# Optimization experiments

Measured on AMD Instinct MI355X. Metric: run time of the kernel, lower is better.

Reference implementation:

```python
import jax, jax.numpy as jnp
import numpy as np

N = 100000
E = 1600000
H = 8
D_IN = 128
D_HEAD = 16  # output_dim // n_heads


def setup_inputs() -> dict:
    key = jax.random.key(0)
    ks = jax.random.split(key, 8)
    x = jax.random.normal(ks[0], (N, D_IN), dtype=jnp.float32)
    W = jax.random.normal(ks[1], (H, D_IN, D_HEAD), dtype=jnp.float32) * 0.05
    a1 = jax.random.normal(ks[2], (H, D_HEAD), dtype=jnp.float32) * 0.1
    b1 = jnp.zeros((H,), dtype=jnp.float32)
    a2 = jax.random.normal(ks[3], (H, D_HEAD), dtype=jnp.float32) * 0.1
    b2 = jnp.zeros((H,), dtype=jnp.float32)
    src = jnp.sort(jax.random.randint(ks[4], (E,), 0, N)).astype(jnp.int32)
    dst = jax.random.randint(ks[5], (E,), 0, N).astype(jnp.int32)
    return {"x": x, "W": W, "a1": a1, "b1": b1, "a2": a2, "b2": b2,
            "src": src, "dst": dst}


def _gat_forward(x, W, a1, b1, a2, b2, src, dst):
    n = x.shape[0]
    # per-head linear transform: [H, N, D_HEAD]
    feats = jnp.einsum('nd,hdo->hno', x, W)
    # per-node attention scalars (1x1 conv with bias): [H, N]
    f1 = jnp.einsum('hno,ho->hn', feats, a1) + b1[:, None]
    f2 = jnp.einsum('hno,ho->hn', feats, a2) + b2[:, None]
    # edge logits: logit[e] = f1[src[e]] + f2[dst[e]]  -> [E, H]
    e = f1[:, src].T + f2[:, dst].T
    e = jnp.maximum(0.2 * e, e)  # leaky_relu
    # sparse row-softmax over each source node's neighbors (segment softmax)
    m = jax.ops.segment_max(e, src, num_segments=n)           # [N, H]
    ex = jnp.exp(e - m[src])                                   # [E, H]
    denom = jax.ops.segment_sum(ex, src, num_segments=n)      # [N, H]
    coef = ex / denom[src]                                     # [E, H]
    # spmm: out[i] = sum_{j in N(i)} coef[ij] * feats[j]
    feats_nhd = jnp.transpose(feats, (1, 0, 2))                # [N, H, D_HEAD]
    msg = coef[:, :, None] * feats_nhd[dst]                    # [E, H, D_HEAD]
    out = jax.ops.segment_sum(msg, src, num_segments=n)       # [N, H, D_HEAD]
    out = out.reshape(n, H * D_HEAD)
    return jax.nn.elu(out)


def reference(x, W, a1, b1, a2, b2, src, dst):
    return _gat_forward(x, W, a1, b1, a2, b2, src, dst)
```

## Files before the change

### kernel.cpp

```cpp
#include <hip/hip_runtime.h>
#include <hip/hip_bf16.h>
#include <math.h>

#define HEADS 8
#define D_IN 128
#define D_HEAD 16
#define D_OUT 128

typedef unsigned short ushort_t;
typedef unsigned int uint_t;
typedef __attribute__((ext_vector_type(8))) short short8;
typedef __attribute__((ext_vector_type(4))) float floatx4;

static __device__ inline uint_t f32_to_bf16(float f) {
    uint_t u = __float_as_uint(f);
    return (u + 0x7fffu + ((u >> 16) & 1u)) >> 16;
}
static __device__ inline uint_t pack_bf16(float lo, float hi) {
    return (f32_to_bf16(hi) << 16) | f32_to_bf16(lo);
}
static __device__ inline float bf_lo(uint_t p) { return __uint_as_float(p << 16); }
static __device__ inline float bf_hi(uint_t p) { return __uint_as_float(p & 0xffff0000u); }

__global__ __launch_bounds__(256) void wprep_kernel(
    const float* __restrict__ Wg, ushort_t* __restrict__ Wbt)
{
    int i = blockIdx.x * 256 + threadIdx.x;
    int c = i >> 7, d = i & 127;
    float v = Wg[(size_t)(c >> 4) * (D_IN * D_HEAD) + d * D_HEAD + (c & 15)];
    Wbt[i] = (ushort_t)f32_to_bf16(v);
}

__global__ __launch_bounds__(256) void gemm_feats_mfma(
    const float* __restrict__ x, const ushort_t* __restrict__ Wbt,
    const float* __restrict__ a1, const float* __restrict__ b1,
    const float* __restrict__ a2, const float* __restrict__ b2,
    ushort_t* __restrict__ feats, float* __restrict__ f1,
    float* __restrict__ f2, int n)
{
    __shared__ ushort_t Xs[64][136];

    const int tid  = threadIdx.x;
    const int wave = tid >> 6;
    const int lane = tid & 63;
    const int row0 = blockIdx.x * 64;

    {
        const int r  = tid >> 2;
        const int c0 = (tid & 3) * 32;
        const bool valid = (row0 + r) < n;
        const float* xr = x + (size_t)(row0 + r) * D_IN + c0;
        uint_t buf[16];
#pragma unroll
        for (int q = 0; q < 8; ++q) {
            float4 v = make_float4(0.f, 0.f, 0.f, 0.f);
            if (valid) v = *(const float4*)(xr + q * 4);
            buf[2 * q]     = pack_bf16(v.x, v.y);
            buf[2 * q + 1] = pack_bf16(v.z, v.w);
        }
        uint4* dp = (uint4*)&Xs[r][c0];
#pragma unroll
        for (int q = 0; q < 4; ++q)
            dp[q] = make_uint4(buf[4 * q], buf[4 * q + 1], buf[4 * q + 2], buf[4 * q + 3]);
    }
    __syncthreads();

    const int m  = lane & 15;
    const int kg = lane >> 4;

    floatx4 acc[8];
#pragma unroll
    for (int ct = 0; ct < 8; ++ct) acc[ct] = (floatx4){0.f, 0.f, 0.f, 0.f};

#pragma unroll
    for (int ks = 0; ks < 4; ++ks) {
        short8 xb = *(const short8*)&Xs[16 * wave + m][ks * 32 + kg * 8];
#pragma unroll
        for (int ct = 0; ct < 8; ++ct) {
            short8 wa = *(const short8*)(Wbt + (size_t)(ct * 16 + m) * D_IN + ks * 32 + kg * 8);
            acc[ct] = __builtin_amdgcn_mfma_f32_16x16x32_bf16(wa, xb, acc[ct], 0, 0, 0);
        }
    }

    const int node = row0 + wave * 16 + m;
    const bool valid = node < n;

    if (valid) {
#pragma unroll
        for (int ct = 0; ct < 8; ++ct) {
            uint_t lo = pack_bf16(acc[ct][0], acc[ct][1]);
            uint_t hi = pack_bf16(acc[ct][2], acc[ct][3]);
            *(uint2*)(feats + (size_t)node * D_OUT + ct * 16 + kg * 4) = make_uint2(lo, hi);
        }
    }

#pragma unroll
    for (int ct = 0; ct < 8; ++ct) {
        float p1 = 0.f, p2 = 0.f;
#pragma unroll
        for (int r = 0; r < 4; ++r) {
            const int o = kg * 4 + r;
            p1 = fmaf(acc[ct][r], a1[ct * D_HEAD + o], p1);
            p2 = fmaf(acc[ct][r], a2[ct * D_HEAD + o], p2);
        }
        p1 += __shfl_xor(p1, 16); p1 += __shfl_xor(p1, 32);
        p2 += __shfl_xor(p2, 16); p2 += __shfl_xor(p2, 32);
        if (kg == 0 && valid) {
            f1[(size_t)node * HEADS + ct] = p1 + b1[ct];
            f2[(size_t)node * HEADS + ct] = p2 + b2[ct];
        }
    }
}

__global__ __launch_bounds__(256) void rowptr_kernel(
    const int* __restrict__ src, int* __restrict__ row_ptr, int n, int e)
{
    int i = blockIdx.x * blockDim.x + threadIdx.x;
    if (i > n) return;
    int lo = 0, hi = e;
    while (lo < hi) {
        int mid = (lo + hi) >> 1;
        if (src[mid] < i) lo = mid + 1; else hi = mid;
    }
    row_ptr[i] = lo;
}

__global__ __launch_bounds__(256) void aggregate_kernel(
    const int* __restrict__ row_ptr, const int* __restrict__ dst,
    const ushort_t* __restrict__ feats,
    const float* __restrict__ f1, const float* __restrict__ f2,
    float* __restrict__ out, int n)
{
    int node = blockIdx.x * 4 + (threadIdx.x >> 6);
    node = __builtin_amdgcn_readfirstlane(node);
    if (node >= n) return;
    const int lane = threadIdx.x & 63;
    const int h = lane >> 3;

    const float f1v   = f1[(size_t)node * HEADS + h];
    const int   start = row_ptr[node];
    const int   end   = row_ptr[node + 1];

    const float*    f2h = f2 + h;
    const ushort_t* fl  = feats + 2 * lane;

    float s = 0.f, ax = 0.f, ay = 0.f;
    int e = start;
    for (; e + 4 <= end; e += 4) {
        const int d0 = dst[e], d1 = dst[e + 1], d2 = dst[e + 2], d3 = dst[e + 3];
        const float g0 = f2h[d0 * HEADS], g1 = f2h[d1 * HEADS];
        const float g2 = f2h[d2 * HEADS], g3 = f2h[d3 * HEADS];
        const uint_t p0 = *(const uint_t*)(fl + d0 * D_OUT);
        const uint_t p1 = *(const uint_t*)(fl + d1 * D_OUT);
        const uint_t p2 = *(const uint_t*)(fl + d2 * D_OUT);
        const uint_t p3 = *(const uint_t*)(fl + d3 * D_OUT);
        float z0 = f1v + g0; z0 = fmaxf(z0, 0.2f * z0);
        float z1 = f1v + g1; z1 = fmaxf(z1, 0.2f * z1);
        float z2 = f1v + g2; z2 = fmaxf(z2, 0.2f * z2);
        float z3 = f1v + g3; z3 = fmaxf(z3, 0.2f * z3);
        const float w0 = __expf(z0), w1 = __expf(z1), w2 = __expf(z2), w3 = __expf(z3);
        s += (w0 + w1) + (w2 + w3);
        ax = fmaf(w0, bf_lo(p0), ax); ay = fmaf(w0, bf_hi(p0), ay);
        ax = fmaf(w1, bf_lo(p1), ax); ay = fmaf(w1, bf_hi(p1), ay);
        ax = fmaf(w2, bf_lo(p2), ax); ay = fmaf(w2, bf_hi(p2), ay);
        ax = fmaf(w3, bf_lo(p3), ax); ay = fmaf(w3, bf_hi(p3), ay);
    }
    for (; e < end; ++e) {
        const int d = dst[e];
        const float g = f2h[d * HEADS];
        const uint_t p = *(const uint_t*)(fl + d * D_OUT);
        float z = f1v + g; z = fmaxf(z, 0.2f * z);
        const float w = __expf(z);
        s += w;
        ax = fmaf(w, bf_lo(p), ax); ay = fmaf(w, bf_hi(p), ay);
    }

    float rx = 0.f, ry = 0.f;
    if (end > start) {
        rx = ax / s;
        ry = ay / s;
        rx = rx > 0.f ? rx : expm1f(rx);
        ry = ry > 0.f ? ry : expm1f(ry);
    }
    *(float2*)(out + (size_t)node * D_OUT + 2 * lane) = make_float2(rx, ry);
}

extern "C" void kernel_launch(void* const* d_in, const int* in_sizes, int n_in,
                              void* d_out, int out_size, void* d_ws, size_t ws_size,
                              hipStream_t stream)
{
    const float* x  = (const float*)d_in[0];
    const float* W  = (const float*)d_in[1];
    const float* a1 = (const float*)d_in[2];
    const float* b1 = (const float*)d_in[3];
    const float* a2 = (const float*)d_in[4];
    const float* b2 = (const float*)d_in[5];
    const int* src  = (const int*)d_in[6];
    const int* dst  = (const int*)d_in[7];
    float* out = (float*)d_out;

    const int n = in_sizes[0] / D_IN;
    const int e = in_sizes[6];

    char* ws = (char*)d_ws;
    size_t off = 0;
    ushort_t* feats = (ushort_t*)(ws + off);
    off += (size_t)n * D_OUT * sizeof(ushort_t); off = (off + 255) & ~(size_t)255;
    float* f1 = (float*)(ws + off);
    off += (size_t)n * HEADS * sizeof(float);    off = (off + 255) & ~(size_t)255;
    float* f2 = (float*)(ws + off);
    off += (size_t)n * HEADS * sizeof(float);    off = (off + 255) & ~(size_t)255;
    int* row_ptr = (int*)(ws + off);
    off += (size_t)(n + 1) * sizeof(int);        off = (off + 255) & ~(size_t)255;
    ushort_t* Wbt = (ushort_t*)(ws + off);

    dim3 blk(256);
    wprep_kernel<<<dim3(64), blk, 0, stream>>>(W, Wbt);
    rowptr_kernel<<<dim3((n + 1 + 255) / 256), blk, 0, stream>>>(src, row_ptr, n, e);
    gemm_feats_mfma<<<dim3((n + 63) / 64), blk, 0, stream>>>(
        x, Wbt, a1, b1, a2, b2, feats, f1, f2, n);
    aggregate_kernel<<<dim3((n + 3) / 4), blk, 0, stream>>>(
        row_ptr, dst, feats, f1, f2, out, n);
}
```

Measured before the change: 239.3 us.

## Merge prep kernels, pre-swizzle W fragments, widen GEMM tile, unroll gather by 8

Merges the weight-conversion and row-pointer kernels into one launch, which saves a kernel launch. W is now stored in MFMA fragment order, so each lane's weight load is one contiguous 16-byte read. The GEMM block now covers 128 rows with two accumulator tiles per wave, so each weight fragment is reused twice; x staging is made fully coalesced and a1/a2 are loaded as float4. The aggregation loop is unrolled to 8 edges to keep more gathers in flight, at the cost of more registers.

Measured after the change: 220.9 us. 1.08x faster.

```diff
diff --git a/kernel.cpp b/kernel.cpp
--- a/kernel.cpp
+++ b/kernel.cpp
@@ -22,107 +22,107 @@
 static __device__ inline float bf_lo(uint_t p) { return __uint_as_float(p << 16); }
 static __device__ inline float bf_hi(uint_t p) { return __uint_as_float(p & 0xffff0000u); }
 
-__global__ __launch_bounds__(256) void wprep_kernel(
-    const float* __restrict__ Wg, ushort_t* __restrict__ Wbt)
-{
-    int i = blockIdx.x * 256 + threadIdx.x;
-    int c = i >> 7, d = i & 127;
-    float v = Wg[(size_t)(c >> 4) * (D_IN * D_HEAD) + d * D_HEAD + (c & 15)];
-    Wbt[i] = (ushort_t)f32_to_bf16(v);
+#define PREP_WBLOCKS 64
+__global__ __launch_bounds__(256) void prep_kernel(
+    const float* __restrict__ Wg, ushort_t* __restrict__ Wfrag,
+    const int* __restrict__ src, int* __restrict__ row_ptr, int n, int e)
+{
+    if (blockIdx.x < PREP_WBLOCKS) {
+        int t = blockIdx.x * 256 + threadIdx.x;
+        int j    = t & 7;
+        int lane = (t >> 3) & 63;
+        int ks   = (t >> 9) & 3;
+        int ct   = t >> 11;
+        int k = ks * 32 + (lane >> 4) * 8 + j;
+        int m = lane & 15;
+        float v = Wg[(size_t)ct * (D_IN * D_HEAD) + k * D_HEAD + m];
+        Wfrag[t] = (ushort_t)f32_to_bf16(v);
+    } else {
+        int i = (blockIdx.x - PREP_WBLOCKS) * 256 + threadIdx.x;
+        if (i > n) return;
+        int lo = 0, hi = e;
+        while (lo < hi) {
+            int mid = (lo + hi) >> 1;
+            if (src[mid] < i) lo = mid + 1; else hi = mid;
+        }
+        row_ptr[i] = lo;
+    }
 }
 
 __global__ __launch_bounds__(256) void gemm_feats_mfma(
-    const float* __restrict__ x, const ushort_t* __restrict__ Wbt,
+    const float* __restrict__ x, const ushort_t* __restrict__ Wfrag,
     const float* __restrict__ a1, const float* __restrict__ b1,
     const float* __restrict__ a2, const float* __restrict__ b2,
     ushort_t* __restrict__ feats, float* __restrict__ f1,
     float* __restrict__ f2, int n)
 {
-    __shared__ ushort_t Xs[64][136];
+    __shared__ ushort_t Xs[128][136];
 
     const int tid  = threadIdx.x;
     const int wave = tid >> 6;
     const int lane = tid & 63;
-    const int row0 = blockIdx.x * 64;
-
-    {
-        const int r  = tid >> 2;
-        const int c0 = (tid & 3) * 32;
-        const bool valid = (row0 + r) < n;
-        const float* xr = x + (size_t)(row0 + r) * D_IN + c0;
-        uint_t buf[16];
-#pragma unroll
-        for (int q = 0; q < 8; ++q) {
-            float4 v = make_float4(0.f, 0.f, 0.f, 0.f);
-            if (valid) v = *(const float4*)(xr + q * 4);
-            buf[2 * q]     = pack_bf16(v.x, v.y);
-            buf[2 * q + 1] = pack_bf16(v.z, v.w);
-        }
-        uint4* dp = (uint4*)&Xs[r][c0];
-#pragma unroll
-        for (int q = 0; q < 4; ++q)
-            dp[q] = make_uint4(buf[4 * q], buf[4 * q + 1], buf[4 * q + 2], buf[4 * q + 3]);
+    const int row0 = blockIdx.x * 128;
+
+#pragma unroll
+    for (int it = 0; it < 16; ++it) {
+        int idx = it * 256 + tid;
+        int r   = idx >> 5;
+        int c4  = (idx & 31) * 4;
+        float4 v = make_float4(0.f, 0.f, 0.f, 0.f);
+        if (row0 + r < n) v = *(const float4*)(x + (size_t)(row0 + r) * D_IN + c4);
+        *(uint2*)&Xs[r][c4] = make_uint2(pack_bf16(v.x, v.y), pack_bf16(v.z, v.w));
     }
     __syncthreads();
 
     const int m  = lane & 15;
     const int kg = lane >> 4;
 
-    floatx4 acc[8];
-#pragma unroll
-    for (int ct = 0; ct < 8; ++ct) acc[ct] = (floatx4){0.f, 0.f, 0.f, 0.f};
+    floatx4 acc[2][8];
+#pragma unroll
+    for (int nt = 0; nt < 2; ++nt)
+#pragma unroll
+        for (int ct = 0; ct < 8; ++ct) acc[nt][ct] = (floatx4){0.f, 0.f, 0.f, 0.f};
 
 #pragma unroll
     for (int ks = 0; ks < 4; ++ks) {
-        short8 xb = *(const short8*)&Xs[16 * wave + m][ks * 32 + kg * 8];
+        short8 xb0 = *(const short8*)&Xs[wave * 32 + m][ks * 32 + kg * 8];
+        short8 xb1 = *(const short8*)&Xs[wave * 32 + 16 + m][ks * 32 + kg * 8];
 #pragma unroll
         for (int ct = 0; ct < 8; ++ct) {
-            short8 wa = *(const short8*)(Wbt + (size_t)(ct * 16 + m) * D_IN + ks * 32 + kg * 8);
-            acc[ct] = __builtin_amdgcn_mfma_f32_16x16x32_bf16(wa, xb, acc[ct], 0, 0, 0);
-        }
-    }
-
-    const int node = row0 + wave * 16 + m;
-    const bool valid = node < n;
-
-    if (valid) {
+            short8 wa = *(const short8*)(Wfrag + ((size_t)(ct * 4 + ks) * 64 + lane) * 8);
+            acc[0][ct] = __builtin_amdgcn_mfma_f32_16x16x32_bf16(wa, xb0, acc[0][ct], 0, 0, 0);
+            acc[1][ct] = __builtin_amdgcn_mfma_f32_16x16x32_bf16(wa, xb1, acc[1][ct], 0, 0, 0);
+        }
+    }
+
+#pragma unroll
+    for (int nt = 0; nt < 2; ++nt) {
+        const int node = row0 + wave * 32 + nt * 16 + m;
+        const bool valid = node < n;
+        if (valid) {
+#pragma unroll
+            for (int ct = 0; ct < 8; ++ct) {
+                uint_t lo = pack_bf16(acc[nt][ct][0], acc[nt][ct][1]);
+                uint_t hi = pack_bf16(acc[nt][ct][2], acc[nt][ct][3]);
+                *(uint2*)(feats + (size_t)node * D_OUT + ct * 16 + kg * 4) = make_uint2(lo, hi);
+            }
+        }
 #pragma unroll
         for (int ct = 0; ct < 8; ++ct) {
-            uint_t lo = pack_bf16(acc[ct][0], acc[ct][1]);
-            uint_t hi = pack_bf16(acc[ct][2], acc[ct][3]);
-            *(uint2*)(feats + (size_t)node * D_OUT + ct * 16 + kg * 4) = make_uint2(lo, hi);
-        }
-    }
-
-#pragma unroll
-    for (int ct = 0; ct < 8; ++ct) {
-        float p1 = 0.f, p2 = 0.f;
-#pragma unroll
-        for (int r = 0; r < 4; ++r) {
-            const int o = kg * 4 + r;
-            p1 = fmaf(acc[ct][r], a1[ct * D_HEAD + o], p1);
-            p2 = fmaf(acc[ct][r], a2[ct * D_HEAD + o], p2);
-        }
-        p1 += __shfl_xor(p1, 16); p1 += __shfl_xor(p1, 32);
-        p2 += __shfl_xor(p2, 16); p2 += __shfl_xor(p2, 32);
-        if (kg == 0 && valid) {
-            f1[(size_t)node * HEADS + ct] = p1 + b1[ct];
-            f2[(size_t)node * HEADS + ct] = p2 + b2[ct];
-        }
-    }
-}
-
-__global__ __launch_bounds__(256) void rowptr_kernel(
-    const int* __restrict__ src, int* __restrict__ row_ptr, int n, int e)
-{
-    int i = blockIdx.x * blockDim.x + threadIdx.x;
-    if (i > n) return;
-    int lo = 0, hi = e;
-    while (lo < hi) {
-        int mid = (lo + hi) >> 1;
-        if (src[mid] < i) lo = mid + 1; else hi = mid;
-    }
-    row_ptr[i] = lo;
+            float4 A1 = *(const float4*)(a1 + ct * D_HEAD + kg * 4);
+            float4 A2 = *(const float4*)(a2 + ct * D_HEAD + kg * 4);
+            float p1 = acc[nt][ct][0] * A1.x + acc[nt][ct][1] * A1.y +
+                       acc[nt][ct][2] * A1.z + acc[nt][ct][3] * A1.w;
+            float p2 = acc[nt][ct][0] * A2.x + acc[nt][ct][1] * A2.y +
+                       acc[nt][ct][2] * A2.z + acc[nt][ct][3] * A2.w;
+            p1 += __shfl_xor(p1, 16); p1 += __shfl_xor(p1, 32);
+            p2 += __shfl_xor(p2, 16); p2 += __shfl_xor(p2, 32);
+            if (kg == 0 && valid) {
+                f1[(size_t)node * HEADS + ct] = p1 + b1[ct];
+                f2[(size_t)node * HEADS + ct] = p2 + b2[ct];
+            }
+        }
+    }
 }
 
 __global__ __launch_bounds__(256) void aggregate_kernel(
@@ -146,33 +146,35 @@
 
     float s = 0.f, ax = 0.f, ay = 0.f;
     int e = start;
-    for (; e + 4 <= end; e += 4) {
-        const int d0 = dst[e], d1 = dst[e + 1], d2 = dst[e + 2], d3 = dst[e + 3];
-        const float g0 = f2h[d0 * HEADS], g1 = f2h[d1 * HEADS];
-        const float g2 = f2h[d2 * HEADS], g3 = f2h[d3 * HEADS];
-        const uint_t p0 = *(const uint_t*)(fl + d0 * D_OUT);
-        const uint_t p1 = *(const uint_t*)(fl + d1 * D_OUT);
-        const uint_t p2 = *(const uint_t*)(fl + d2 * D_OUT);
-        const uint_t p3 = *(const uint_t*)(fl + d3 * D_OUT);
-        float z0 = f1v + g0; z0 = fmaxf(z0, 0.2f * z0);
-        float z1 = f1v + g1; z1 = fmaxf(z1, 0.2f * z1);
-        float z2 = f1v + g2; z2 = fmaxf(z2, 0.2f * z2);
-        float z3 = f1v + g3; z3 = fmaxf(z3, 0.2f * z3);
-        const float w0 = __expf(z0), w1 = __expf(z1), w2 = __expf(z2), w3 = __expf(z3);
-        s += (w0 + w1) + (w2 + w3);
-        ax = fmaf(w0, bf_lo(p0), ax); ay = fmaf(w0, bf_hi(p0), ay);
-        ax = fmaf(w1, bf_lo(p1), ax); ay = fmaf(w1, bf_hi(p1), ay);
-        ax = fmaf(w2, bf_lo(p2), ax); ay = fmaf(w2, bf_hi(p2), ay);
-        ax = fmaf(w3, bf_lo(p3), ax); ay = fmaf(w3, bf_hi(p3), ay);
+    for (; e + 8 <= end; e += 8) {
+        int d[8]; float g[8]; uint_t p[8];
+#pragma unroll
+        for (int q = 0; q < 8; ++q) d[q] = dst[e + q];
+#pragma unroll
+        for (int q = 0; q < 8; ++q) {
+            g[q] = f2h[d[q] * HEADS];
+            p[q] = *(const uint_t*)(fl + d[q] * D_OUT);
+        }
+#pragma unroll
+        for (int q = 0; q < 8; ++q) {
+            float z = f1v + g[q];
+            z = fmaxf(z, 0.2f * z);
+            float w = __expf(z);
+            s += w;
+            ax = fmaf(w, bf_lo(p[q]), ax);
+            ay = fmaf(w, bf_hi(p[q]), ay);
+        }
     }
     for (; e < end; ++e) {
         const int d = dst[e];
         const float g = f2h[d * HEADS];
         const uint_t p = *(const uint_t*)(fl + d * D_OUT);
-        float z = f1v + g; z = fmaxf(z, 0.2f * z);
+        float z = f1v + g;
+        z = fmaxf(z, 0.2f * z);
         const float w = __expf(z);
         s += w;
-        ax = fmaf(w, bf_lo(p), ax); ay = fmaf(w, bf_hi(p), ay);
+        ax = fmaf(w, bf_lo(p), ax);
+        ay = fmaf(w, bf_hi(p), ay);
     }
 
     float rx = 0.f, ry = 0.f;
@@ -212,13 +214,14 @@
     off += (size_t)n * HEADS * sizeof(float);    off = (off + 255) & ~(size_t)255;
     int* row_ptr = (int*)(ws + off);
     off += (size_t)(n + 1) * sizeof(int);        off = (off + 255) & ~(size_t)255;
-    ushort_t* Wbt = (ushort_t*)(ws + off);
+    ushort_t* Wfrag = (ushort_t*)(ws + off);
 
     dim3 blk(256);
-    wprep_kernel<<<dim3(64), blk, 0, stream>>>(W, Wbt);
-    rowptr_kernel<<<dim3((n + 1 + 255) / 256), blk, 0, stream>>>(src, row_ptr, n, e);
-    gemm_feats_mfma<<<dim3((n + 63) / 64), blk, 0, stream>>>(
-        x, Wbt, a1, b1, a2, b2, feats, f1, f2, n);
+    const int rp_blocks = (n + 1 + 255) / 256;
+    prep_kernel<<<dim3(PREP_WBLOCKS + rp_blocks), blk, 0, stream>>>(
+        W, Wfrag, src, row_ptr, n, e);
+    gemm_feats_mfma<<<dim3((n + 127) / 128), blk, 0, stream>>>(
+        x, Wfrag, a1, b1, a2, b2, feats, f1, f2, n);
     aggregate_kernel<<<dim3((n + 3) / 4), blk, 0, stream>>>(
         row_ptr, dst, feats, f1, f2, out, n);
 }
```
